# Kernel optimization log

Hardware: AMD Instinct MI355X
Metric: run time of the kernel (lower is better)

## Reference

```python
import jax, jax.numpy as jnp
import numpy as np

N_NODES = 100000


def _gcn_conv(x, edge_index, W, b, n):
    """PyG GCNConv: h = x @ W; add self-loops; symmetric deg^-1/2 norm; scatter-add; + b."""
    h = x @ W                                            # [N, F_out]
    src = jnp.concatenate([edge_index[0], jnp.arange(n)])  # self-loops appended
    dst = jnp.concatenate([edge_index[1], jnp.arange(n)])
    deg = jax.ops.segment_sum(jnp.ones_like(dst, dtype=h.dtype), dst, num_segments=n)
    dinv = jnp.where(deg > 0, jax.lax.rsqrt(deg), 0.0)   # deg^-1/2 with inf->0
    norm = dinv[src] * dinv[dst]                         # [E+N]
    msg = h[src] * norm[:, None]                         # gather + scale
    out = jax.ops.segment_sum(msg, dst, num_segments=n)  # scatter-add
    return out + b


def setup_inputs() -> dict:
    key = jax.random.key(0)
    ks = jax.random.split(key, 4)
    x = jax.random.normal(ks[0], (N_NODES, 128), dtype=jnp.float32)
    edge_index = jax.random.randint(ks[1], (2, 1600000), 0, N_NODES, dtype=jnp.int64)
    W1 = jax.random.normal(ks[2], (128, 128), dtype=jnp.float32) * (1.0 / np.sqrt(128))
    b1 = jnp.zeros((128,), dtype=jnp.float32)
    W2 = jax.random.normal(ks[3], (128, 16), dtype=jnp.float32) * (1.0 / np.sqrt(128))
    b2 = jnp.zeros((16,), dtype=jnp.float32)
    return {"x": x, "edge_index": edge_index, "W1": W1, "b1": b1, "W2": W2, "b2": b2}


def reference(x, edge_index, W1, b1, W2, b2):
    n = x.shape[0]
    h = jax.nn.relu(_gcn_conv(x, edge_index, W1, b1, n))
    out = _gcn_conv(h, edge_index, W2, b2, n)
    return out
```

## Files before the change

kernel.cpp:

```cpp
#include <hip/hip_runtime.h>
#include <hip/hip_bf16.h>

typedef __attribute__((ext_vector_type(8))) short bf16x8;
typedef __attribute__((ext_vector_type(4))) float f32x4;

#define ELL_W 64
#define BSH   8
#define BCAP  4608
#define CHUNK 4096


__device__ __forceinline__ float bf2f(unsigned short u) {
    return __uint_as_float(((unsigned int)u) << 16);
}
__device__ __forceinline__ unsigned short f2bf(float f) {
    unsigned int u = __float_as_uint(f);
    unsigned int r = (u + 0x7fffu + ((u >> 16) & 1u)) >> 16;
    return (unsigned short)r;
}

__global__ void zero_kernel(int* __restrict__ a, int n) {
    int i = blockIdx.x * blockDim.x + threadIdx.x;
    if (i < n) a[i] = 0;
}


__global__ __launch_bounds__(256) void p1_partition_kernel(const int* __restrict__ ei, int E, int N, int NB,
                                                           int* __restrict__ gcur, int* __restrict__ bucket) {
    __shared__ int hist[512];
    __shared__ int gbase[512];
    __shared__ int cur2[512];
    int tid = threadIdx.x;
    int c0 = blockIdx.x * CHUNK;

    for (int i = tid; i < NB; i += 256) { hist[i] = 0; cur2[i] = 0; }
    __syncthreads();

    int rec[16], bkt[16];
#pragma unroll
    for (int k = 0; k < 16; ++k) {
        int e = c0 + k * 256 + tid;
        int b = -1, r = 0;
        if (e < E) {
            int s = ei[e], d = ei[E + e];
            if ((unsigned)s < (unsigned)N && (unsigned)d < (unsigned)N) {
                b = d >> BSH;
                r = (s << BSH) | (d & ((1 << BSH) - 1));
            }
        }
        bkt[k] = b; rec[k] = r;
        if (b >= 0) atomicAdd(&hist[b], 1);
    }
    __syncthreads();

    for (int i = tid; i < NB; i += 256) {
        int c = hist[i];
        gbase[i] = (c > 0) ? atomicAdd(&gcur[i * 16], c) : 0;
    }
    __syncthreads();

#pragma unroll
    for (int k = 0; k < 16; ++k) {
        int b = bkt[k];
        if (b >= 0) {
            int r = atomicAdd(&cur2[b], 1);
            int pos = gbase[b] + r;
            if (pos < BCAP) bucket[(size_t)b * BCAP + pos] = rec[k];
        }
    }
}


__global__ __launch_bounds__(256) void p2_ell_kernel(const int* __restrict__ bucket,
                                                     const int* __restrict__ gcur, int N,
                                                     int* __restrict__ cursor, int* __restrict__ ell) {
    int b = blockIdx.x;
    int cnt = gcur[b * 16]; if (cnt > BCAP) cnt = BCAP;
    const int* reg = &bucket[(size_t)b * BCAP];
    for (int k = threadIdx.x; k < cnt; k += 256) {
        int rec = reg[k];
        int s = (int)(((unsigned)rec) >> BSH);
        int dst = (b << BSH) | (rec & ((1 << BSH) - 1));
        if (dst < N) {
            int pos = atomicAdd(&cursor[dst], 1);
            if (pos < ELL_W) ell[(size_t)dst * ELL_W + pos] = s;
        }
    }
}


__global__ void pad_kernel(const int* __restrict__ deg, int N,
                           int* __restrict__ ell, unsigned short* __restrict__ h1) {
    int i = blockIdx.x * blockDim.x + threadIdx.x;
    if (i < 128) h1[(size_t)N * 128 + i] = 0;
    if (i < N) {
        int d = deg[i]; if (d > ELL_W) d = ELL_W;
        int d4 = (d + 3) & ~3; if (d4 > ELL_W) d4 = ELL_W;
        for (int k = d; k < d4; ++k) ell[(size_t)i * ELL_W + k] = N;
    }
}

__global__ void compute_dinv_kernel(const int* __restrict__ deg, float* __restrict__ dinv, int N) {
    int i = blockIdx.x * blockDim.x + threadIdx.x;
    if (i < N) dinv[i] = rsqrtf((float)(deg[i] + 1));
}


__global__ void build_wfrag_kernel(const float* __restrict__ W1, unsigned short* __restrict__ wfrag) {
    int t = blockIdx.x * blockDim.x + threadIdx.x;
    if (t >= 2048) return;
    int ln = t & 63;
    int blk = t >> 6;
    int j = blk >> 2, k0 = blk & 3;
    int nn = ln & 15, cc = ln >> 4;
    int n = j * 16 + nn;
    unsigned short tmp[8];
#pragma unroll
    for (int i = 0; i < 8; ++i) {
        int k = k0 * 32 + cc * 8 + i;
        tmp[i] = f2bf(W1[(size_t)k * 128 + n]);
    }
    *(uint4*)&wfrag[(size_t)t * 8] = *(const uint4*)tmp;
}


__global__ __launch_bounds__(256) void gemm1_mfma_kernel(const float* __restrict__ X,
                                                         const unsigned short* __restrict__ wfrag,
                                                         const float* __restrict__ dinv,
                                                         unsigned short* __restrict__ H, int N) {
    __shared__ __align__(16) unsigned short wl[16384];
    int tid = threadIdx.x;
    {
        uint4* dst = (uint4*)wl;
        const uint4* src = (const uint4*)wfrag;
        for (int idx = tid; idx < 2048; idx += 256) dst[idx] = src[idx];
    }
    __syncthreads();

    int lane = tid & 63;
    int wave = tid >> 6;
    int m0 = blockIdx.x * 128 + wave * 32;
    int mrow = lane & 15;
    int kc = lane >> 4;

    f32x4 acc[2][8];
#pragma unroll
    for (int rt = 0; rt < 2; ++rt)
#pragma unroll
        for (int j = 0; j < 8; ++j) acc[rt][j] = (f32x4)(0.f);

#pragma unroll
    for (int k0 = 0; k0 < 4; ++k0) {
        bf16x8 a[2];
#pragma unroll
        for (int rt = 0; rt < 2; ++rt) {
            int row = m0 + rt * 16 + mrow;
            bf16x8 av = (bf16x8)(short)0;
            if (row < N) {
                const float4* p = (const float4*)&X[(size_t)row * 128 + k0 * 32 + kc * 8];
                float4 v0 = p[0], v1 = p[1];
                av[0] = (short)f2bf(v0.x); av[1] = (short)f2bf(v0.y);
                av[2] = (short)f2bf(v0.z); av[3] = (short)f2bf(v0.w);
                av[4] = (short)f2bf(v1.x); av[5] = (short)f2bf(v1.y);
                av[6] = (short)f2bf(v1.z); av[7] = (short)f2bf(v1.w);
            }
            a[rt] = av;
        }
#pragma unroll
        for (int j = 0; j < 8; ++j) {
            bf16x8 b = *(const bf16x8*)&wl[((size_t)(j * 4 + k0) * 64 + lane) * 8];
            acc[0][j] = __builtin_amdgcn_mfma_f32_16x16x32_bf16(a[0], b, acc[0][j], 0, 0, 0);
            acc[1][j] = __builtin_amdgcn_mfma_f32_16x16x32_bf16(a[1], b, acc[1][j], 0, 0, 0);
        }
    }

#pragma unroll
    for (int rt = 0; rt < 2; ++rt) {
#pragma unroll
        for (int r = 0; r < 4; ++r) {
            int row = m0 + rt * 16 + 4 * kc + r;
            if (row < N) {
                float dv = dinv[row];
#pragma unroll
                for (int j = 0; j < 8; ++j) {
                    H[(size_t)row * 128 + j * 16 + mrow] = f2bf(dv * acc[rt][j][r]);
                }
            }
        }
    }
}


__global__ __launch_bounds__(256) void agg128_fused_kernel(const unsigned short* __restrict__ H,
                                                           const int* __restrict__ ell,
                                                           const int* __restrict__ deg,
                                                           const float* __restrict__ dinv,
                                                           const float* __restrict__ b1,
                                                           const float* __restrict__ W2,
                                                           unsigned short* __restrict__ h2out, int N) {
    __shared__ float gbuf[4][128];
    int lane = threadIdx.x & 63;
    int w = threadIdx.x >> 6;
    int i0 = blockIdx.x * 16 + w * 4;

    int n = lane & 15;
    int q = lane >> 4;
    int sub = lane >> 5;
    int fl = lane & 31;

    float w2r[32];
#pragma unroll
    for (int m = 0; m < 32; ++m) {
        int mm = (m + 8 * q) & 31;
        w2r[m] = W2[(size_t)(q * 32 + mm) * 16 + n];
    }

    for (int nn = 0; nn < 4; ++nn) {
        int i = i0 + nn;
        if (i >= N) break;
        int d = deg[i]; if (d > ELL_W) d = ELL_W;
        int d4 = (d + 3) & ~3; if (d4 > ELL_W) d4 = ELL_W;
        float di = dinv[i];

        ushort4 hv = *(const ushort4*)&H[(size_t)i * 128 + 4 * fl];
        float a0 = sub ? 0.f : bf2f(hv.x);
        float a1 = sub ? 0.f : bf2f(hv.y);
        float a2 = sub ? 0.f : bf2f(hv.z);
        float a3 = sub ? 0.f : bf2f(hv.w);

        const int* row = &ell[(size_t)i * ELL_W];
        for (int e = 0; e < d4; e += 4) {
            int4 sv = *(const int4*)&row[e];
            int sA = sub ? sv.y : sv.x;
            int sB = sub ? sv.w : sv.z;
            ushort4 gA = *(const ushort4*)&H[(size_t)sA * 128 + 4 * fl];
            ushort4 gB = *(const ushort4*)&H[(size_t)sB * 128 + 4 * fl];
            a0 += bf2f(gA.x) + bf2f(gB.x);
            a1 += bf2f(gA.y) + bf2f(gB.y);
            a2 += bf2f(gA.z) + bf2f(gB.z);
            a3 += bf2f(gA.w) + bf2f(gB.w);
        }

        a0 += __shfl_xor(a0, 32, 64);
        a1 += __shfl_xor(a1, 32, 64);
        a2 += __shfl_xor(a2, 32, 64);
        a3 += __shfl_xor(a3, 32, 64);

        if (sub == 0) {
            float4 bb = *(const float4*)&b1[4 * fl];
            float4 gv;
            gv.x = fmaxf(di * a0 + bb.x, 0.f);
            gv.y = fmaxf(di * a1 + bb.y, 0.f);
            gv.z = fmaxf(di * a2 + bb.z, 0.f);
            gv.w = fmaxf(di * a3 + bb.w, 0.f);
            *(float4*)&gbuf[w][4 * fl] = gv;
        }
        asm volatile("s_waitcnt lgkmcnt(0)" ::: "memory");

        float partial = 0.f;
#pragma unroll
        for (int t = 0; t < 8; ++t) {
            int off = (t * 4 + 8 * q) & 31;
            float4 gv = *(const float4*)&gbuf[w][q * 32 + off];
            partial += gv.x * w2r[t * 4 + 0] + gv.y * w2r[t * 4 + 1] +
                       gv.z * w2r[t * 4 + 2] + gv.w * w2r[t * 4 + 3];
        }
        partial += __shfl_xor(partial, 16, 64);
        partial += __shfl_xor(partial, 32, 64);
        if (lane < 16) h2out[(size_t)i * 16 + lane] = f2bf(di * partial);
    }
}


__global__ __launch_bounds__(256) void agg16_kernel(const unsigned short* __restrict__ H,
                                                    const int* __restrict__ ell,
                                                    const int* __restrict__ deg,
                                                    const float* __restrict__ dinv,
                                                    const float* __restrict__ b2,
                                                    float* __restrict__ out, int N) {
    int lane = threadIdx.x & 63;
    int i = blockIdx.x * 4 + (threadIdx.x >> 6);
    if (i >= N) return;
    int t = lane & 15;
    int q = lane >> 4;

    int d = deg[i]; if (d > ELL_W) d = ELL_W;
    float di = dinv[i];
    const int* row = &ell[(size_t)i * ELL_W];

    float partial = (q == 0) ? bf2f(H[(size_t)i * 16 + t]) : 0.f;
#pragma unroll 2
    for (int e = q; e < d; e += 4) {
        int s = row[e];
        partial += bf2f(H[(size_t)s * 16 + t]);
    }
    partial += __shfl_xor(partial, 16, 64);
    partial += __shfl_xor(partial, 32, 64);
    if (lane < 16) out[(size_t)i * 16 + t] = di * partial + b2[t];
}


extern "C" void kernel_launch(void* const* d_in, const int* in_sizes, int n_in,
                              void* d_out, int out_size, void* d_ws, size_t ws_size,
                              hipStream_t stream) {
    const float* x = (const float*)d_in[0];
    const int* ei = (const int*)d_in[1];
    const float* W1 = (const float*)d_in[2];
    const float* b1 = (const float*)d_in[3];
    const float* W2 = (const float*)d_in[4];
    const float* b2 = (const float*)d_in[5];
    float* out = (float*)d_out;

    const int N = in_sizes[0] / 128;
    const int E = in_sizes[1] / 2;
    const int NB = (N + (1 << BSH) - 1) >> BSH;

    char* base = (char*)d_ws;
    size_t off = 0;
    auto align_up = [](size_t v) { return (v + 255) & ~(size_t)255; };

    int* cursor = (int*)(base + off);                      off = align_up(off + (size_t)N * 4);
    float* dinv = (float*)(base + off);                    off = align_up(off + (size_t)N * 4);
    int* ell = (int*)(base + off);                         off = align_up(off + (size_t)N * ELL_W * 4);
    int* gcur = (int*)(base + off);                        off = align_up(off + (size_t)NB * 16 * 4);
    int* bucket = (int*)(base + off);                      off = align_up(off + (size_t)NB * BCAP * 4);
    unsigned short* wfrag = (unsigned short*)(base + off); off = align_up(off + (size_t)16384 * 2);
    unsigned short* h1 = (unsigned short*)(base + off);    off = align_up(off + (size_t)(N + 1) * 128 * 2);
    unsigned short* h2 = (unsigned short*)(base + off);    off = align_up(off + (size_t)N * 16 * 2);

    zero_kernel<<<(N + 255) / 256, 256, 0, stream>>>(cursor, N);
    zero_kernel<<<(NB * 16 + 255) / 256, 256, 0, stream>>>(gcur, NB * 16);
    build_wfrag_kernel<<<8, 256, 0, stream>>>(W1, wfrag);

    int nchunks = (E + CHUNK - 1) / CHUNK;
    p1_partition_kernel<<<nchunks, 256, 0, stream>>>(ei, E, N, NB, gcur, bucket);
    p2_ell_kernel<<<NB, 256, 0, stream>>>(bucket, gcur, N, cursor, ell);
    pad_kernel<<<(N + 255) / 256, 256, 0, stream>>>(cursor, N, ell, h1);
    compute_dinv_kernel<<<(N + 255) / 256, 256, 0, stream>>>(cursor, dinv, N);

    gemm1_mfma_kernel<<<(N + 127) / 128, 256, 0, stream>>>(x, wfrag, dinv, h1, N);
    agg128_fused_kernel<<<(N + 15) / 16, 256, 0, stream>>>(h1, ell, cursor, dinv, b1, W2, h2, N);
    agg16_kernel<<<(N + 3) / 4, 256, 0, stream>>>(h2, ell, cursor, dinv, b2, out, N);
}
```

Measured before the change: 214.5 us.

## Widen gather loads, pad ELL rows to 8, and split partition/ELL build across more blocks

```diff
diff --git a/kernel.cpp b/kernel.cpp
--- a/kernel.cpp
+++ b/kernel.cpp
@@ -3,11 +3,13 @@
 
 typedef __attribute__((ext_vector_type(8))) short bf16x8;
 typedef __attribute__((ext_vector_type(4))) float f32x4;
+typedef __attribute__((ext_vector_type(8))) unsigned short u16x8;
 
 #define ELL_W 64
 #define BSH   8
 #define BCAP  4608
-#define CHUNK 4096
+#define CHUNK 1024
+#define PSPLIT 4
 
 
 __device__ __forceinline__ float bf2f(unsigned short u) {
@@ -17,6 +19,11 @@
     unsigned int u = __float_as_uint(f);
     unsigned int r = (u + 0x7fffu + ((u >> 16) & 1u)) >> 16;
     return (unsigned short)r;
+}
+__device__ __forceinline__ int sel4(int sub, int4 v) {
+    int s = (sub & 1) ? v.y : v.x;
+    int t = (sub & 1) ? v.w : v.z;
+    return (sub & 2) ? t : s;
 }
 
 __global__ void zero_kernel(int* __restrict__ a, int n) {
@@ -36,9 +43,9 @@
     for (int i = tid; i < NB; i += 256) { hist[i] = 0; cur2[i] = 0; }
     __syncthreads();
 
-    int rec[16], bkt[16];
-#pragma unroll
-    for (int k = 0; k < 16; ++k) {
+    int rec[4], bkt[4];
+#pragma unroll
+    for (int k = 0; k < 4; ++k) {
         int e = c0 + k * 256 + tid;
         int b = -1, r = 0;
         if (e < E) {
@@ -60,7 +67,7 @@
     __syncthreads();
 
 #pragma unroll
-    for (int k = 0; k < 16; ++k) {
+    for (int k = 0; k < 4; ++k) {
         int b = bkt[k];
         if (b >= 0) {
             int r = atomicAdd(&cur2[b], 1);
@@ -74,10 +81,14 @@
 __global__ __launch_bounds__(256) void p2_ell_kernel(const int* __restrict__ bucket,
                                                      const int* __restrict__ gcur, int N,
                                                      int* __restrict__ cursor, int* __restrict__ ell) {
-    int b = blockIdx.x;
+    int b = blockIdx.x / PSPLIT;
+    int seg = blockIdx.x % PSPLIT;
     int cnt = gcur[b * 16]; if (cnt > BCAP) cnt = BCAP;
+    int per = (cnt + PSPLIT - 1) / PSPLIT;
+    int k0 = seg * per;
+    int k1 = min(k0 + per, cnt);
     const int* reg = &bucket[(size_t)b * BCAP];
-    for (int k = threadIdx.x; k < cnt; k += 256) {
+    for (int k = k0 + threadIdx.x; k < k1; k += 256) {
         int rec = reg[k];
         int s = (int)(((unsigned)rec) >> BSH);
         int dst = (b << BSH) | (rec & ((1 << BSH) - 1));
@@ -90,13 +101,15 @@
 
 
 __global__ void pad_kernel(const int* __restrict__ deg, int N,
-                           int* __restrict__ ell, unsigned short* __restrict__ h1) {
+                           int* __restrict__ ell, unsigned short* __restrict__ h1,
+                           unsigned short* __restrict__ h2) {
     int i = blockIdx.x * blockDim.x + threadIdx.x;
     if (i < 128) h1[(size_t)N * 128 + i] = 0;
+    if (i < 16) h2[(size_t)N * 16 + i] = 0;
     if (i < N) {
         int d = deg[i]; if (d > ELL_W) d = ELL_W;
-        int d4 = (d + 3) & ~3; if (d4 > ELL_W) d4 = ELL_W;
-        for (int k = d; k < d4; ++k) ell[(size_t)i * ELL_W + k] = N;
+        int d8 = (d + 7) & ~7; if (d8 > ELL_W) d8 = ELL_W;
+        for (int k = d; k < d8; ++k) ell[(size_t)i * ELL_W + k] = N;
     }
 }
 
@@ -205,8 +218,8 @@
 
     int n = lane & 15;
     int q = lane >> 4;
-    int sub = lane >> 5;
-    int fl = lane & 31;
+    int sub = lane >> 4;
+    int fl = lane & 15;
 
     float w2r[32];
 #pragma unroll
@@ -219,41 +232,60 @@
         int i = i0 + nn;
         if (i >= N) break;
         int d = deg[i]; if (d > ELL_W) d = ELL_W;
-        int d4 = (d + 3) & ~3; if (d4 > ELL_W) d4 = ELL_W;
+        int d8 = (d + 7) & ~7; if (d8 > ELL_W) d8 = ELL_W;
         float di = dinv[i];
 
-        ushort4 hv = *(const ushort4*)&H[(size_t)i * 128 + 4 * fl];
-        float a0 = sub ? 0.f : bf2f(hv.x);
-        float a1 = sub ? 0.f : bf2f(hv.y);
-        float a2 = sub ? 0.f : bf2f(hv.z);
-        float a3 = sub ? 0.f : bf2f(hv.w);
+        float a0, a1, a2, a3, a4, a5, a6, a7;
+        {
+            u16x8 hv = *(const u16x8*)&H[(size_t)i * 128 + 8 * fl];
+            bool z = (sub != 0);
+            a0 = z ? 0.f : bf2f(hv[0]); a1 = z ? 0.f : bf2f(hv[1]);
+            a2 = z ? 0.f : bf2f(hv[2]); a3 = z ? 0.f : bf2f(hv[3]);
+            a4 = z ? 0.f : bf2f(hv[4]); a5 = z ? 0.f : bf2f(hv[5]);
+            a6 = z ? 0.f : bf2f(hv[6]); a7 = z ? 0.f : bf2f(hv[7]);
+        }
 
         const int* row = &ell[(size_t)i * ELL_W];
-        for (int e = 0; e < d4; e += 4) {
-            int4 sv = *(const int4*)&row[e];
-            int sA = sub ? sv.y : sv.x;
-            int sB = sub ? sv.w : sv.z;
-            ushort4 gA = *(const ushort4*)&H[(size_t)sA * 128 + 4 * fl];
-            ushort4 gB = *(const ushort4*)&H[(size_t)sB * 128 + 4 * fl];
-            a0 += bf2f(gA.x) + bf2f(gB.x);
-            a1 += bf2f(gA.y) + bf2f(gB.y);
-            a2 += bf2f(gA.z) + bf2f(gB.z);
-            a3 += bf2f(gA.w) + bf2f(gB.w);
-        }
-
-        a0 += __shfl_xor(a0, 32, 64);
-        a1 += __shfl_xor(a1, 32, 64);
-        a2 += __shfl_xor(a2, 32, 64);
-        a3 += __shfl_xor(a3, 32, 64);
+        for (int e = 0; e < d8; e += 8) {
+            int4 svA = *(const int4*)&row[e];
+            int4 svB = *(const int4*)&row[e + 4];
+            int sA = sel4(sub, svA);
+            int sB = sel4(sub, svB);
+            u16x8 gA = *(const u16x8*)&H[(size_t)sA * 128 + 8 * fl];
+            u16x8 gB = *(const u16x8*)&H[(size_t)sB * 128 + 8 * fl];
+            a0 += bf2f(gA[0]) + bf2f(gB[0]);
+            a1 += bf2f(gA[1]) + bf2f(gB[1]);
+            a2 += bf2f(gA[2]) + bf2f(gB[2]);
+            a3 += bf2f(gA[3]) + bf2f(gB[3]);
+            a4 += bf2f(gA[4]) + bf2f(gB[4]);
+            a5 += bf2f(gA[5]) + bf2f(gB[5]);
+            a6 += bf2f(gA[6]) + bf2f(gB[6]);
+            a7 += bf2f(gA[7]) + bf2f(gB[7]);
+        }
+
+        a0 += __shfl_xor(a0, 32, 64); a0 += __shfl_xor(a0, 16, 64);
+        a1 += __shfl_xor(a1, 32, 64); a1 += __shfl_xor(a1, 16, 64);
+        a2 += __shfl_xor(a2, 32, 64); a2 += __shfl_xor(a2, 16, 64);
+        a3 += __shfl_xor(a3, 32, 64); a3 += __shfl_xor(a3, 16, 64);
+        a4 += __shfl_xor(a4, 32, 64); a4 += __shfl_xor(a4, 16, 64);
+        a5 += __shfl_xor(a5, 32, 64); a5 += __shfl_xor(a5, 16, 64);
+        a6 += __shfl_xor(a6, 32, 64); a6 += __shfl_xor(a6, 16, 64);
+        a7 += __shfl_xor(a7, 32, 64); a7 += __shfl_xor(a7, 16, 64);
 
         if (sub == 0) {
-            float4 bb = *(const float4*)&b1[4 * fl];
-            float4 gv;
-            gv.x = fmaxf(di * a0 + bb.x, 0.f);
-            gv.y = fmaxf(di * a1 + bb.y, 0.f);
-            gv.z = fmaxf(di * a2 + bb.z, 0.f);
-            gv.w = fmaxf(di * a3 + bb.w, 0.f);
-            *(float4*)&gbuf[w][4 * fl] = gv;
+            float4 bb0 = *(const float4*)&b1[8 * fl];
+            float4 bb1 = *(const float4*)&b1[8 * fl + 4];
+            float4 g0, g1;
+            g0.x = fmaxf(di * a0 + bb0.x, 0.f);
+            g0.y = fmaxf(di * a1 + bb0.y, 0.f);
+            g0.z = fmaxf(di * a2 + bb0.z, 0.f);
+            g0.w = fmaxf(di * a3 + bb0.w, 0.f);
+            g1.x = fmaxf(di * a4 + bb1.x, 0.f);
+            g1.y = fmaxf(di * a5 + bb1.y, 0.f);
+            g1.z = fmaxf(di * a6 + bb1.z, 0.f);
+            g1.w = fmaxf(di * a7 + bb1.w, 0.f);
+            *(float4*)&gbuf[w][8 * fl] = g0;
+            *(float4*)&gbuf[w][8 * fl + 4] = g1;
         }
         asm volatile("s_waitcnt lgkmcnt(0)" ::: "memory");
 
@@ -281,22 +313,42 @@
     int lane = threadIdx.x & 63;
     int i = blockIdx.x * 4 + (threadIdx.x >> 6);
     if (i >= N) return;
-    int t = lane & 15;
-    int q = lane >> 4;
+    int fl = lane & 7;
+    int sub = lane >> 3;
 
     int d = deg[i]; if (d > ELL_W) d = ELL_W;
+    int d8 = (d + 7) & ~7; if (d8 > ELL_W) d8 = ELL_W;
     float di = dinv[i];
     const int* row = &ell[(size_t)i * ELL_W];
 
-    float partial = (q == 0) ? bf2f(H[(size_t)i * 16 + t]) : 0.f;
-#pragma unroll 2
-    for (int e = q; e < d; e += 4) {
-        int s = row[e];
-        partial += bf2f(H[(size_t)s * 16 + t]);
-    }
-    partial += __shfl_xor(partial, 16, 64);
-    partial += __shfl_xor(partial, 32, 64);
-    if (lane < 16) out[(size_t)i * 16 + t] = di * partial + b2[t];
+    float a0, a1;
+    {
+        ushort2 hv = *(const ushort2*)&H[(size_t)i * 16 + 2 * fl];
+        bool z = (sub != 0);
+        a0 = z ? 0.f : bf2f(hv.x);
+        a1 = z ? 0.f : bf2f(hv.y);
+    }
+
+    for (int e = 0; e < d8; e += 8) {
+        int4 svA = *(const int4*)&row[e];
+        int4 svB = *(const int4*)&row[e + 4];
+        int sA_ = sel4(sub & 3, svA);
+        int sB_ = sel4(sub & 3, svB);
+        int s = (sub & 4) ? sB_ : sA_;
+        ushort2 g = *(const ushort2*)&H[(size_t)s * 16 + 2 * fl];
+        a0 += bf2f(g.x);
+        a1 += bf2f(g.y);
+    }
+
+    a0 += __shfl_xor(a0, 32, 64); a0 += __shfl_xor(a0, 16, 64); a0 += __shfl_xor(a0, 8, 64);
+    a1 += __shfl_xor(a1, 32, 64); a1 += __shfl_xor(a1, 16, 64); a1 += __shfl_xor(a1, 8, 64);
+
+    if (lane < 8) {
+        float2 o;
+        o.x = di * a0 + b2[2 * fl];
+        o.y = di * a1 + b2[2 * fl + 1];
+        *(float2*)&out[(size_t)i * 16 + 2 * fl] = o;
+    }
 }
 
 
@@ -326,7 +378,7 @@
     int* bucket = (int*)(base + off);                      off = align_up(off + (size_t)NB * BCAP * 4);
     unsigned short* wfrag = (unsigned short*)(base + off); off = align_up(off + (size_t)16384 * 2);
     unsigned short* h1 = (unsigned short*)(base + off);    off = align_up(off + (size_t)(N + 1) * 128 * 2);
-    unsigned short* h2 = (unsigned short*)(base + off);    off = align_up(off + (size_t)N * 16 * 2);
+    unsigned short* h2 = (unsigned short*)(base + off);    off = align_up(off + (size_t)(N + 1) * 16 * 2);
 
     zero_kernel<<<(N + 255) / 256, 256, 0, stream>>>(cursor, N);
     zero_kernel<<<(NB * 16 + 255) / 256, 256, 0, stream>>>(gcur, NB * 16);
@@ -334,8 +386,8 @@
 
     int nchunks = (E + CHUNK - 1) / CHUNK;
     p1_partition_kernel<<<nchunks, 256, 0, stream>>>(ei, E, N, NB, gcur, bucket);
-    p2_ell_kernel<<<NB, 256, 0, stream>>>(bucket, gcur, N, cursor, ell);
-    pad_kernel<<<(N + 255) / 256, 256, 0, stream>>>(cursor, N, ell, h1);
+    p2_ell_kernel<<<NB * PSPLIT, 256, 0, stream>>>(bucket, gcur, N, cursor, ell);
+    pad_kernel<<<(N + 255) / 256, 256, 0, stream>>>(cursor, N, ell, h1, h2);
     compute_dinv_kernel<<<(N + 255) / 256, 256, 0, stream>>>(cursor, dinv, N);
 
     gemm1_mfma_kernel<<<(N + 127) / 128, 256, 0, stream>>>(x, wfrag, dinv, h1, N);
```

Measured after the change: 253.8 us. +18.3%, slower.
